# Kernel tuning notes

Measured on AMD Instinct MI355X. Metric: run time of the kernel, lower is better.

Reference implementation:

```python
import math
import jax, jax.numpy as jnp
import numpy as np

B, T, C, H = 4, 1024, 1024, 16
HD = C // H
BLOCK = 1024


def setup_inputs() -> dict:
    key = jax.random.key(0)
    k0, k1, k2, k3 = jax.random.split(key, 4)
    x = jax.random.normal(k0, (B, T, C), dtype=jnp.float32)
    # torch Linear weight is (out, in); we store (in, out) and apply x @ W + b
    W_attn = jax.random.normal(k1, (C, 3 * C), dtype=jnp.float32) * 0.02
    b_attn = jnp.zeros((3 * C,), dtype=jnp.float32)
    W_proj = jax.random.normal(k2, (C, C), dtype=jnp.float32) * 0.02
    b_proj = jnp.zeros((C,), dtype=jnp.float32)
    # rel_pos_emb: (n_head, block_size, head_dim), std 0.02 (leading 1 dim dropped)
    rel_pos_emb = jax.random.normal(k3, (H, BLOCK, HD), dtype=jnp.float32) * 0.02
    return {"x": x, "W_attn": W_attn, "b_attn": b_attn,
            "W_proj": W_proj, "b_proj": b_proj, "rel_pos_emb": rel_pos_emb}


def reference(x, W_attn, b_attn, W_proj, b_proj, rel_pos_emb):
    Bx, Tx, Cx = x.shape
    qkv = x @ W_attn + b_attn                      # (B, T, 3C)
    q, k, v = jnp.split(qkv, 3, axis=2)
    q = q.reshape(Bx, Tx, H, HD).transpose(0, 2, 1, 3)   # (B, H, T, hd)
    k = k.reshape(Bx, Tx, H, HD).transpose(0, 2, 1, 3)
    v = v.reshape(Bx, Tx, H, HD).transpose(0, 2, 1, 3)

    att = jnp.einsum('bhid,bhjd->bhij', q, k)      # (B, H, T, T)

    # relative position score: pos[b,h,i,j] = sum_d E[h, clamp(i-j,0), d] * k[b,h,j,d]
    # compute P[b,h,r,j] = <E[h,r,:], k[b,h,j,:]> then gather r = clamp(i-j, 0)
    rng = jnp.arange(Tx)
    dist = jnp.clip(rng[:, None] - rng[None, :], 0, None)          # (T, T)
    P = jnp.einsum('hrd,bhjd->bhrj', rel_pos_emb[:, :Tx], k)       # (B, H, T, T)
    pos_score = jnp.take_along_axis(P, dist[None, None, :, :], axis=2)
    att = att + pos_score

    att = att * (1.0 / math.sqrt(HD))
    causal = jnp.tril(jnp.ones((Tx, Tx), dtype=bool))
    att = jnp.where(causal[None, None], att, -jnp.inf)
    att = jax.nn.softmax(att, axis=-1)
    # dropout p=0.0 -> identity
    y = jnp.einsum('bhij,bhjd->bhid', att, v)      # (B, H, T, hd)
    y = y.transpose(0, 2, 1, 3).reshape(Bx, Tx, Cx)
    return y @ W_proj + b_proj
```

## Files before the change

### kernel.cpp

```cpp
#include <hip/hip_runtime.h>


typedef __bf16 bf16x8 __attribute__((ext_vector_type(8)));
typedef float f32x4 __attribute__((ext_vector_type(4)));
typedef unsigned short ushort_t;

#define T_SEQ 1024
#define NHEAD 16
#define HDIM 64
#define PLANE 4194304

__device__ __forceinline__ float bf2f(ushort_t h) {
    unsigned int u = ((unsigned int)h) << 16;
    float f; __builtin_memcpy(&f, &u, 4); return f;
}
__device__ __forceinline__ ushort_t f2bf(float f) {
    __bf16 h = (__bf16)f;
    ushort_t u; __builtin_memcpy(&u, &h, 2); return u;
}

__global__ __launch_bounds__(256) void sentinel_kernel(float* out, int n, float val) {
    const int i = blockIdx.x * 256 + threadIdx.x;
    if (i < n) out[i] = val;
}

__global__ __launch_bounds__(256) void convert2(
    const float* __restrict__ x, ushort_t* __restrict__ x16,
    const float* __restrict__ E, ushort_t* __restrict__ E16)
{
    const int bid = blockIdx.x;
    const float* src; ushort_t* dst; int base;
    if (bid < 4096) { src = x; dst = x16; base = bid * 1024; }
    else            { src = E; dst = E16; base = (bid - 4096) * 1024; }
    const int i = base + (int)threadIdx.x * 4;
    const float4 v = *reinterpret_cast<const float4*>(src + i);
    union { unsigned long long u; ushort_t s[4]; } o;
    o.s[0] = f2bf(v.x); o.s[1] = f2bf(v.y); o.s[2] = f2bf(v.z); o.s[3] = f2bf(v.w);
    *reinterpret_cast<unsigned long long*>(dst + i) = o.u;
}

__global__ __launch_bounds__(256) void transpose_bf16(
    const float* __restrict__ W, ushort_t* __restrict__ Wt, int Kdim, int Ndim)
{
    __shared__ ushort_t t[64][65];
    const int n0 = blockIdx.x * 64, k0 = blockIdx.y * 64;
    const int cx = threadIdx.x & 63, ry = threadIdx.x >> 6;
#pragma unroll
    for (int i = 0; i < 16; i++) {
        const int r = ry + i * 4;
        t[r][cx] = f2bf(W[(size_t)(k0 + r) * Ndim + n0 + cx]);
    }
    __syncthreads();
#pragma unroll
    for (int i = 0; i < 16; i++) {
        const int r = ry + i * 4;
        Wt[(size_t)(n0 + r) * Kdim + k0 + cx] = t[cx][r];
    }
}

__global__ __launch_bounds__(256) void transpose_v(
    const ushort_t* __restrict__ v, ushort_t* __restrict__ vT)
{
    __shared__ ushort_t t[64][65];
    const int bh = blockIdx.y;
    const int t0 = blockIdx.x * 64;
    const int cx = threadIdx.x & 63, ry = threadIdx.x >> 6;
    const ushort_t* src = v + (size_t)bh * 65536;
    ushort_t* dst = vT + (size_t)bh * 65536;
#pragma unroll
    for (int i = 0; i < 16; i++) {
        const int r = ry + i * 4;
        t[r][cx] = src[(size_t)(t0 + r) * HDIM + cx];
    }
    __syncthreads();
#pragma unroll
    for (int i = 0; i < 16; i++) {
        const int d = ry + i * 4;
        dst[(size_t)d * T_SEQ + t0 + cx] = t[cx][d];
    }
}

template <int MODE>
__global__ __launch_bounds__(256) void gemm128(
    const ushort_t* __restrict__ A16, const ushort_t* __restrict__ Bt,
    const float* __restrict__ bias, void* __restrict__ out_,
    int Ndim, int Kdim)
{
    __shared__ __align__(16) ushort_t As[128 * 32];
    __shared__ __align__(16) ushort_t Bs[128 * 32];

    const int tid = threadIdx.x;
    const int w = tid >> 6;
    const int lane = tid & 63;
    const int l15 = lane & 15;
    const int quad = lane >> 4;
    const int m0 = blockIdx.y * 128, n0 = blockIdx.x * 128;
    const int wm = (w & 1) * 64, wn = (w >> 1) * 64;

    f32x4 acc[4][4];
#pragma unroll
    for (int mt = 0; mt < 4; mt++)
#pragma unroll
        for (int nt = 0; nt < 4; nt++) acc[mt][nt] = (f32x4){0.f, 0.f, 0.f, 0.f};

    for (int kk = 0; kk < Kdim; kk += 32) {
        __syncthreads();
#pragma unroll
        for (int t = 0; t < 2; t++) {
            const int chunk = w * 128 + t * 64 + lane;
            const int row = chunk >> 2, kc = (chunk & 3) * 8;
            __builtin_amdgcn_global_load_lds(
                (const __attribute__((address_space(1))) void*)
                    (A16 + (size_t)(m0 + row) * Kdim + kk + kc),
                (__attribute__((address_space(3))) void*)
                    (As + (size_t)(w * 128 + t * 64) * 8), 16, 0, 0);
            __builtin_amdgcn_global_load_lds(
                (const __attribute__((address_space(1))) void*)
                    (Bt + (size_t)(n0 + row) * Kdim + kk + kc),
                (__attribute__((address_space(3))) void*)
                    (Bs + (size_t)(w * 128 + t * 64) * 8), 16, 0, 0);
        }
        __syncthreads();

        bf16x8 af[4], bf[4];
#pragma unroll
        for (int mt = 0; mt < 4; mt++)
            af[mt] = *reinterpret_cast<const bf16x8*>(&As[(wm + mt * 16 + l15) * 32 + quad * 8]);
#pragma unroll
        for (int nt = 0; nt < 4; nt++)
            bf[nt] = *reinterpret_cast<const bf16x8*>(&Bs[(wn + nt * 16 + l15) * 32 + quad * 8]);
#pragma unroll
        for (int mt = 0; mt < 4; mt++)
#pragma unroll
            for (int nt = 0; nt < 4; nt++)
                acc[mt][nt] = __builtin_amdgcn_mfma_f32_16x16x32_bf16(
                    af[mt], bf[nt], acc[mt][nt], 0, 0, 0);
    }

#pragma unroll
    for (int mt = 0; mt < 4; mt++)
#pragma unroll
        for (int nt = 0; nt < 4; nt++) {
            const int n = n0 + wn + nt * 16 + l15;
            const float bv = bias[n];
#pragma unroll
            for (int r = 0; r < 4; r++) {
                const int m = m0 + wm + mt * 16 + quad * 4 + r;
                const float val = acc[mt][nt][r] + bv;
                if (MODE == 0) {
                    ushort_t* ws = (ushort_t*)out_;
                    const int which = n >> 10;
                    const size_t pl = (which == 2) ? 3 : which;
                    const int cc = n & 1023;
                    const int h = cc >> 6, d = cc & 63;
                    const int bb = m >> 10, t = m & 1023;
                    ws[pl * PLANE + ((size_t)(bb * NHEAD + h) * T_SEQ + t) * HDIM + d] = f2bf(val);
                } else {
                    ((float*)out_)[(size_t)m * Ndim + n] = val;
                }
            }
        }
}

__global__ __launch_bounds__(256) void flash_attn(
    const ushort_t* __restrict__ qp, const ushort_t* __restrict__ kp,
    const ushort_t* __restrict__ vTp, const ushort_t* __restrict__ E16,
    ushort_t* __restrict__ y16)
{
    __shared__ __align__(16) ushort_t Ks[64 * 72];
    __shared__ __align__(16) ushort_t Vt[64 * 72];
    __shared__ __align__(16) ushort_t Es[128 * 72];
    __shared__ __align__(16) ushort_t Ps[64 * 68 + 16];

    const int bh = blockIdx.x;
    const int h = bh & (NHEAD - 1);
    const int b = bh >> 4;
    const int it = 15 - (int)blockIdx.y;
    const int tid = threadIdx.x;
    const int w = tid >> 6;
    const int lane = tid & 63;
    const int l15 = lane & 15;
    const int quad = lane >> 4;

    const size_t base = (size_t)bh * T_SEQ * HDIM;
    const ushort_t* Eh = E16 + (size_t)h * T_SEQ * HDIM;
    const ushort_t* vTb = vTp + (size_t)bh * 65536;
    const float c1 = 0.125f * 1.44269504f;

    const int rq = tid >> 2, cq = (tid & 3) * 16;
    const int re = tid >> 1, ce = (tid & 1) * 32;

    const int kosz = ((l15 >> 3) & 1) << 3;
    const int pswz = ((quad >> 1) & 1) << 3;
    const int l15p = l15 ^ pswz;
    const int eswz = ((re >> 3) & 1) << 3;

    bf16x8 ones;
#pragma unroll
    for (int i = 0; i < 8; i++) ones[i] = (__bf16)1.0f;

    const int i0 = it * 64;

    bf16x8 qf[2];
    {
        const ushort_t* qrow = qp + base + (size_t)(i0 + w * 16 + l15) * HDIM;
        qf[0] = *reinterpret_cast<const bf16x8*>(qrow + quad * 8);
        qf[1] = *reinterpret_cast<const bf16x8*>(qrow + 32 + quad * 8);
    }

    f32x4 o[4], o5;
#pragma unroll
    for (int dt = 0; dt < 4; dt++) o[dt] = (f32x4){0.f, 0.f, 0.f, 0.f};
    o5 = (f32x4){0.f, 0.f, 0.f, 0.f};
    float mrow[4];
#pragma unroll
    for (int r = 0; r < 4; r++) mrow[r] = -3e38f;

    for (int j0 = 0; j0 <= i0; j0 += 64) {
        const int d0 = i0 - j0;
        __syncthreads();
        {
            const ushort_t* ksrc = kp + base + (size_t)(j0 + rq) * HDIM + cq;
            *reinterpret_cast<uint4*>(&Ks[rq * 72 + cq]) = *reinterpret_cast<const uint4*>(ksrc);
            *reinterpret_cast<uint4*>(&Ks[rq * 72 + cq + 8]) = *reinterpret_cast<const uint4*>(ksrc + 8);
            const ushort_t* vsrc = vTb + (size_t)rq * T_SEQ + j0 + cq;
            *reinterpret_cast<uint4*>(&Vt[rq * 72 + cq]) = *reinterpret_cast<const uint4*>(vsrc);
            *reinterpret_cast<uint4*>(&Vt[rq * 72 + cq + 8]) = *reinterpret_cast<const uint4*>(vsrc + 8);
        }
        {
            int g = d0 - 64 + re;
            g = g < 0 ? 0 : (g > 1023 ? 1023 : g);
            const ushort_t* esrc = Eh + (size_t)g * HDIM + ce;
#pragma unroll
            for (int q16 = 0; q16 < 4; q16++)
                *reinterpret_cast<uint4*>(&Es[re * 72 + ce + ((q16 * 8) ^ eswz)]) =
                    *reinterpret_cast<const uint4*>(esrc + q16 * 8);
        }
        __syncthreads();

        f32x4 s[4], pb[2][4];
#pragma unroll
        for (int nt = 0; nt < 4; nt++) {
            s[nt] = (f32x4){0.f, 0.f, 0.f, 0.f};
            pb[0][nt] = (f32x4){0.f, 0.f, 0.f, 0.f};
            pb[1][nt] = (f32x4){0.f, 0.f, 0.f, 0.f};
        }
#pragma unroll
        for (int ks = 0; ks < 2; ks++) {
            const int ko = ks * 32 + quad * 8;
            const bf16x8 ae0 = *reinterpret_cast<const bf16x8*>(&Es[(w * 32 + l15) * 72 + (ko ^ kosz)]);
            const bf16x8 ae1 = *reinterpret_cast<const bf16x8*>(&Es[(w * 32 + 16 + l15) * 72 + (ko ^ kosz)]);
#pragma unroll
            for (int nt = 0; nt < 4; nt++) {
                const bf16x8 bk = *reinterpret_cast<const bf16x8*>(&Ks[(nt * 16 + l15) * 72 + ko]);
                s[nt] = __builtin_amdgcn_mfma_f32_16x16x32_bf16(qf[ks], bk, s[nt], 0, 0, 0);
                pb[0][nt] = __builtin_amdgcn_mfma_f32_16x16x32_bf16(ae0, bk, pb[0][nt], 0, 0, 0);
                pb[1][nt] = __builtin_amdgcn_mfma_f32_16x16x32_bf16(ae1, bk, pb[1][nt], 0, 0, 0);
            }
        }
#pragma unroll
        for (int mf = 0; mf < 2; mf++)
#pragma unroll
            for (int nt = 0; nt < 4; nt++) {
                const int jl = nt * 16 + l15;
#pragma unroll
                for (int r = 0; r < 4; r++) {
                    const int br = w * 32 + mf * 16 + quad * 4 + r;
                    const int il_t = br - 64 + jl;
                    const int addr = ((unsigned)il_t < 64u) ? il_t * 68 + jl : 4352;
                    Ps[addr] = f2bf(pb[mf][nt][r]);
                }
            }
        __syncthreads();

        float pv[4][4], mnew[4];
#pragma unroll
        for (int r = 0; r < 4; r++) mnew[r] = mrow[r];
        const int il0 = w * 16 + quad * 4;
        if (j0 < i0) {
#pragma unroll
            for (int nt = 0; nt < 4; nt++) {
                const int jl = nt * 16 + l15;
#pragma unroll
                for (int r = 0; r < 4; r++) {
                    const float sv = (s[nt][r] + bf2f(Ps[(il0 + r) * 68 + jl])) * c1;
                    pv[nt][r] = sv;
                    mnew[r] = fmaxf(mnew[r], sv);
                }
            }
        } else {
#pragma unroll
            for (int nt = 0; nt < 4; nt++) {
                const int jl = nt * 16 + l15;
#pragma unroll
                for (int r = 0; r < 4; r++) {
                    const int il = il0 + r;
                    float sv = (s[nt][r] + bf2f(Ps[il * 68 + jl])) * c1;
                    if (jl > il) sv = -3e38f;
                    pv[nt][r] = sv;
                    mnew[r] = fmaxf(mnew[r], sv);
                }
            }
        }
#pragma unroll
        for (int r = 0; r < 4; r++)
#pragma unroll
            for (int off = 1; off < 16; off <<= 1)
                mnew[r] = fmaxf(mnew[r], __shfl_xor(mnew[r], off, 64));
        float alpha[4];
#pragma unroll
        for (int r = 0; r < 4; r++) {
            alpha[r] = exp2f(mrow[r] - mnew[r]);
            mrow[r] = mnew[r];
        }
#pragma unroll
        for (int nt = 0; nt < 4; nt++)
#pragma unroll
            for (int r = 0; r < 4; r++)
                pv[nt][r] = exp2f(pv[nt][r] - mnew[r]);
#pragma unroll
        for (int dt = 0; dt < 4; dt++)
#pragma unroll
            for (int r = 0; r < 4; r++) o[dt][r] *= alpha[r];
#pragma unroll
        for (int r = 0; r < 4; r++) o5[r] *= alpha[r];
#pragma unroll
        for (int nt = 0; nt < 4; nt++)
#pragma unroll
            for (int r = 0; r < 4; r++)
                Es[(w * 16 + quad * 4 + r) * 72 + nt * 16 + l15p] = f2bf(pv[nt][r]);

#pragma unroll
        for (int ks = 0; ks < 2; ks++) {
            const int ko = ks * 32 + quad * 8;
            const bf16x8 ap = *reinterpret_cast<const bf16x8*>(&Es[(w * 16 + l15) * 72 + (ko ^ kosz)]);
#pragma unroll
            for (int dt = 0; dt < 4; dt++) {
                const bf16x8 bv = *reinterpret_cast<const bf16x8*>(&Vt[(dt * 16 + l15) * 72 + ko]);
                o[dt] = __builtin_amdgcn_mfma_f32_16x16x32_bf16(ap, bv, o[dt], 0, 0, 0);
            }
            o5 = __builtin_amdgcn_mfma_f32_16x16x32_bf16(ap, ones, o5, 0, 0, 0);
        }
    }

    float inv[4];
#pragma unroll
    for (int r = 0; r < 4; r++) inv[r] = 1.0f / o5[r];
#pragma unroll
    for (int dt = 0; dt < 4; dt++)
#pragma unroll
        for (int r = 0; r < 4; r++) {
            const int il = w * 16 + quad * 4 + r;
            const int d = dt * 16 + l15;
            y16[((size_t)(b * T_SEQ + i0 + il)) * 1024 + h * 64 + d] = f2bf(o[dt][r] * inv[r]);
        }
}

extern "C" void kernel_launch(void* const* d_in, const int* in_sizes, int n_in,
                              void* d_out, int out_size, void* d_ws, size_t ws_size,
                              hipStream_t stream) {
    float* out = (float*)d_out;

    const void* x = nullptr; const void* Wa = nullptr; const void* ba = nullptr;
    const void* Wp = nullptr; const void* bp = nullptr; const void* E = nullptr;
    int anomaly = 0;
    if (n_in != 6) {
        anomaly = 2;
    } else {
        int c1M = 0;
        for (int i = 0; i < 6; i++) {
            const int s = in_sizes[i];
            if      (s == 4194304) x  = d_in[i];
            else if (s == 3145728) Wa = d_in[i];
            else if (s == 3072)    ba = d_in[i];
            else if (s == 1024)    bp = d_in[i];
            else if (s == 1048576) { if (c1M == 0) Wp = d_in[i]; else E = d_in[i]; c1M++; }
            else anomaly = 1;
        }
        if (!x || !Wa || !ba || !Wp || !bp || !E || c1M != 2) anomaly = 1;
    }
    if (!anomaly && out_size != 4194304) anomaly = 3;
    if (!anomaly && ws_size < (size_t)52428800) anomaly = 4;
    if (anomaly) {
        sentinel_kernel<<<(out_size + 255) / 256, 256, 0, stream>>>(out, out_size, 1000.0f * anomaly);
        return;
    }

    ushort_t* ws   = (ushort_t*)d_ws;
    ushort_t* qp   = ws;
    ushort_t* kp   = ws + (size_t)PLANE;
    ushort_t* vTp  = ws + (size_t)2 * PLANE;
    ushort_t* vtmp = ws + (size_t)3 * PLANE;
    ushort_t* y16  = vtmp;
    ushort_t* x16  = ws + (size_t)4 * PLANE;
    ushort_t* WaT  = ws + (size_t)5 * PLANE;
    ushort_t* WpT  = WaT + (size_t)3145728;
    ushort_t* E16  = WpT + (size_t)1048576;

    convert2<<<5120, 256, 0, stream>>>((const float*)x, x16, (const float*)E, E16);
    transpose_bf16<<<dim3(48, 16), 256, 0, stream>>>((const float*)Wa, WaT, 1024, 3072);
    transpose_bf16<<<dim3(16, 16), 256, 0, stream>>>((const float*)Wp, WpT, 1024, 1024);

    gemm128<0><<<dim3(24, 32), 256, 0, stream>>>(x16, WaT, (const float*)ba, (void*)ws, 3072, 1024);

    transpose_v<<<dim3(16, 64), 256, 0, stream>>>(vtmp, vTp);

    flash_attn<<<dim3(64, 16), 256, 0, stream>>>(qp, kp, vTp, E16, y16);

    gemm128<1><<<dim3(8, 32), 256, 0, stream>>>(y16, WpT, (const float*)bp, (void*)out, 1024, 1024);
}
```

Before: 219.1 us.

## Fuse prep kernels, swizzle attention LDS, narrow projection GEMM tiles, add setprio

Merges the three weight and activation conversion kernels into a single prep launch. In flash attention it replaces padded LDS strides (72/68) with unpadded 64-wide rows using XOR swizzles, and reuses the Ks buffer for the probability tile. It also adds s_setprio around the MFMA sections and a launch_bounds occupancy hint of 4. The output projection GEMM switches to 128x64 tiles so that 512 blocks are launched instead of 256. These changes aim to cut launch overhead, LDS footprint and bank conflicts, and to raise occupancy, at the risk of swizzle-index mistakes and register pressure.

```diff
diff --git a/kernel.cpp b/kernel.cpp
--- a/kernel.cpp
+++ b/kernel.cpp
@@ -24,26 +24,35 @@
     if (i < n) out[i] = val;
 }
 
-__global__ __launch_bounds__(256) void convert2(
+__global__ __launch_bounds__(256) void prep(
     const float* __restrict__ x, ushort_t* __restrict__ x16,
-    const float* __restrict__ E, ushort_t* __restrict__ E16)
-{
-    const int bid = blockIdx.x;
-    const float* src; ushort_t* dst; int base;
-    if (bid < 4096) { src = x; dst = x16; base = bid * 1024; }
-    else            { src = E; dst = E16; base = (bid - 4096) * 1024; }
-    const int i = base + (int)threadIdx.x * 4;
-    const float4 v = *reinterpret_cast<const float4*>(src + i);
-    union { unsigned long long u; ushort_t s[4]; } o;
-    o.s[0] = f2bf(v.x); o.s[1] = f2bf(v.y); o.s[2] = f2bf(v.z); o.s[3] = f2bf(v.w);
-    *reinterpret_cast<unsigned long long*>(dst + i) = o.u;
-}
-
-__global__ __launch_bounds__(256) void transpose_bf16(
-    const float* __restrict__ W, ushort_t* __restrict__ Wt, int Kdim, int Ndim)
+    const float* __restrict__ E, ushort_t* __restrict__ E16,
+    const float* __restrict__ Wa, ushort_t* __restrict__ WaT,
+    const float* __restrict__ Wp, ushort_t* __restrict__ WpT)
 {
     __shared__ ushort_t t[64][65];
-    const int n0 = blockIdx.x * 64, k0 = blockIdx.y * 64;
+    const int bid = blockIdx.x;
+    if (bid < 5120) {
+        const float* src; ushort_t* dst; int base;
+        if (bid < 4096) { src = x; dst = x16; base = bid * 1024; }
+        else            { src = E; dst = E16; base = (bid - 4096) * 1024; }
+        const int i = base + (int)threadIdx.x * 4;
+        const float4 v = *reinterpret_cast<const float4*>(src + i);
+        union { unsigned long long u; ushort_t s[4]; } o;
+        o.s[0] = f2bf(v.x); o.s[1] = f2bf(v.y); o.s[2] = f2bf(v.z); o.s[3] = f2bf(v.w);
+        *reinterpret_cast<unsigned long long*>(dst + i) = o.u;
+        return;
+    }
+    const float* W; ushort_t* Wt; int Kdim, Ndim, n0, k0;
+    if (bid < 5888) {
+        const int r = bid - 5120;
+        W = Wa; Wt = WaT; Kdim = 1024; Ndim = 3072;
+        n0 = (r % 48) * 64; k0 = (r / 48) * 64;
+    } else {
+        const int r = bid - 5888;
+        W = Wp; Wt = WpT; Kdim = 1024; Ndim = 1024;
+        n0 = (r % 16) * 64; k0 = (r / 16) * 64;
+    }
     const int cx = threadIdx.x & 63, ry = threadIdx.x >> 6;
 #pragma unroll
     for (int i = 0; i < 16; i++) {
@@ -80,28 +89,29 @@
     }
 }
 
-template <int MODE>
+template <int MODE, int BN>
 __global__ __launch_bounds__(256) void gemm128(
     const ushort_t* __restrict__ A16, const ushort_t* __restrict__ Bt,
     const float* __restrict__ bias, void* __restrict__ out_,
     int Ndim, int Kdim)
 {
+    constexpr int NT = BN / 32;
     __shared__ __align__(16) ushort_t As[128 * 32];
-    __shared__ __align__(16) ushort_t Bs[128 * 32];
+    __shared__ __align__(16) ushort_t Bs[BN * 32];
 
     const int tid = threadIdx.x;
     const int w = tid >> 6;
     const int lane = tid & 63;
     const int l15 = lane & 15;
     const int quad = lane >> 4;
-    const int m0 = blockIdx.y * 128, n0 = blockIdx.x * 128;
-    const int wm = (w & 1) * 64, wn = (w >> 1) * 64;
-
-    f32x4 acc[4][4];
+    const int m0 = blockIdx.y * 128, n0 = blockIdx.x * BN;
+    const int wm = (w & 1) * 64, wn = (w >> 1) * (BN / 2);
+
+    f32x4 acc[4][NT];
 #pragma unroll
     for (int mt = 0; mt < 4; mt++)
 #pragma unroll
-        for (int nt = 0; nt < 4; nt++) acc[mt][nt] = (f32x4){0.f, 0.f, 0.f, 0.f};
+        for (int nt = 0; nt < NT; nt++) acc[mt][nt] = (f32x4){0.f, 0.f, 0.f, 0.f};
 
     for (int kk = 0; kk < Kdim; kk += 32) {
         __syncthreads();
@@ -114,25 +124,35 @@
                     (A16 + (size_t)(m0 + row) * Kdim + kk + kc),
                 (__attribute__((address_space(3))) void*)
                     (As + (size_t)(w * 128 + t * 64) * 8), 16, 0, 0);
+            if (BN == 128)
+                __builtin_amdgcn_global_load_lds(
+                    (const __attribute__((address_space(1))) void*)
+                        (Bt + (size_t)(n0 + row) * Kdim + kk + kc),
+                    (__attribute__((address_space(3))) void*)
+                        (Bs + (size_t)(w * 128 + t * 64) * 8), 16, 0, 0);
+        }
+        if (BN == 64) {
+            const int chunk = w * 64 + lane;
+            const int row = chunk >> 2, kc = (chunk & 3) * 8;
             __builtin_amdgcn_global_load_lds(
                 (const __attribute__((address_space(1))) void*)
                     (Bt + (size_t)(n0 + row) * Kdim + kk + kc),
                 (__attribute__((address_space(3))) void*)
-                    (Bs + (size_t)(w * 128 + t * 64) * 8), 16, 0, 0);
+                    (Bs + (size_t)(w * 64) * 8), 16, 0, 0);
         }
         __syncthreads();
 
-        bf16x8 af[4], bf[4];
+        bf16x8 af[4], bf[NT];
 #pragma unroll
         for (int mt = 0; mt < 4; mt++)
             af[mt] = *reinterpret_cast<const bf16x8*>(&As[(wm + mt * 16 + l15) * 32 + quad * 8]);
 #pragma unroll
-        for (int nt = 0; nt < 4; nt++)
+        for (int nt = 0; nt < NT; nt++)
             bf[nt] = *reinterpret_cast<const bf16x8*>(&Bs[(wn + nt * 16 + l15) * 32 + quad * 8]);
 #pragma unroll
         for (int mt = 0; mt < 4; mt++)
 #pragma unroll
-            for (int nt = 0; nt < 4; nt++)
+            for (int nt = 0; nt < NT; nt++)
                 acc[mt][nt] = __builtin_amdgcn_mfma_f32_16x16x32_bf16(
                     af[mt], bf[nt], acc[mt][nt], 0, 0, 0);
     }
@@ -140,7 +160,7 @@
 #pragma unroll
     for (int mt = 0; mt < 4; mt++)
 #pragma unroll
-        for (int nt = 0; nt < 4; nt++) {
+        for (int nt = 0; nt < NT; nt++) {
             const int n = n0 + wn + nt * 16 + l15;
             const float bv = bias[n];
 #pragma unroll
@@ -162,15 +182,15 @@
         }
 }
 
-__global__ __launch_bounds__(256) void flash_attn(
+__global__ __launch_bounds__(256, 4) void flash_attn(
     const ushort_t* __restrict__ qp, const ushort_t* __restrict__ kp,
     const ushort_t* __restrict__ vTp, const ushort_t* __restrict__ E16,
     ushort_t* __restrict__ y16)
 {
-    __shared__ __align__(16) ushort_t Ks[64 * 72];
-    __shared__ __align__(16) ushort_t Vt[64 * 72];
-    __shared__ __align__(16) ushort_t Es[128 * 72];
-    __shared__ __align__(16) ushort_t Ps[64 * 68 + 16];
+    __shared__ __align__(16) ushort_t Ks[64 * 64];
+    __shared__ __align__(16) ushort_t Vt[64 * 64];
+    __shared__ __align__(16) ushort_t Es[128 * 64];
+    __shared__ __align__(16) ushort_t Ps[64 * 64];
 
     const int bh = blockIdx.x;
     const int h = bh & (NHEAD - 1);
@@ -190,10 +210,10 @@
     const int rq = tid >> 2, cq = (tid & 3) * 16;
     const int re = tid >> 1, ce = (tid & 1) * 32;
 
-    const int kosz = ((l15 >> 3) & 1) << 3;
-    const int pswz = ((quad >> 1) & 1) << 3;
-    const int l15p = l15 ^ pswz;
-    const int eswz = ((re >> 3) & 1) << 3;
+    const int kswz = (l15 & 7) << 3;
+    const int swr  = (rq & 7) << 3;
+    const int swe  = (re & 7) << 3;
+    const int jswz = quad << 4;
 
     bf16x8 ones;
 #pragma unroll
@@ -221,11 +241,11 @@
         __syncthreads();
         {
             const ushort_t* ksrc = kp + base + (size_t)(j0 + rq) * HDIM + cq;
-            *reinterpret_cast<uint4*>(&Ks[rq * 72 + cq]) = *reinterpret_cast<const uint4*>(ksrc);
-            *reinterpret_cast<uint4*>(&Ks[rq * 72 + cq + 8]) = *reinterpret_cast<const uint4*>(ksrc + 8);
+            *reinterpret_cast<uint4*>(&Ks[rq * 64 + (cq ^ swr)]) = *reinterpret_cast<const uint4*>(ksrc);
+            *reinterpret_cast<uint4*>(&Ks[rq * 64 + ((cq + 8) ^ swr)]) = *reinterpret_cast<const uint4*>(ksrc + 8);
             const ushort_t* vsrc = vTb + (size_t)rq * T_SEQ + j0 + cq;
-            *reinterpret_cast<uint4*>(&Vt[rq * 72 + cq]) = *reinterpret_cast<const uint4*>(vsrc);
-            *reinterpret_cast<uint4*>(&Vt[rq * 72 + cq + 8]) = *reinterpret_cast<const uint4*>(vsrc + 8);
+            *reinterpret_cast<uint4*>(&Vt[rq * 64 + (cq ^ swr)]) = *reinterpret_cast<const uint4*>(vsrc);
+            *reinterpret_cast<uint4*>(&Vt[rq * 64 + ((cq + 8) ^ swr)]) = *reinterpret_cast<const uint4*>(vsrc + 8);
         }
         {
             int g = d0 - 64 + re;
@@ -233,7 +253,7 @@
             const ushort_t* esrc = Eh + (size_t)g * HDIM + ce;
 #pragma unroll
             for (int q16 = 0; q16 < 4; q16++)
-                *reinterpret_cast<uint4*>(&Es[re * 72 + ce + ((q16 * 8) ^ eswz)]) =
+                *reinterpret_cast<uint4*>(&Es[re * 64 + ((ce + q16 * 8) ^ swe)]) =
                     *reinterpret_cast<const uint4*>(esrc + q16 * 8);
         }
         __syncthreads();
@@ -245,19 +265,21 @@
             pb[0][nt] = (f32x4){0.f, 0.f, 0.f, 0.f};
             pb[1][nt] = (f32x4){0.f, 0.f, 0.f, 0.f};
         }
+        __builtin_amdgcn_s_setprio(1);
 #pragma unroll
         for (int ks = 0; ks < 2; ks++) {
             const int ko = ks * 32 + quad * 8;
-            const bf16x8 ae0 = *reinterpret_cast<const bf16x8*>(&Es[(w * 32 + l15) * 72 + (ko ^ kosz)]);
-            const bf16x8 ae1 = *reinterpret_cast<const bf16x8*>(&Es[(w * 32 + 16 + l15) * 72 + (ko ^ kosz)]);
+            const bf16x8 ae0 = *reinterpret_cast<const bf16x8*>(&Es[(w * 32 + l15) * 64 + (ko ^ kswz)]);
+            const bf16x8 ae1 = *reinterpret_cast<const bf16x8*>(&Es[(w * 32 + 16 + l15) * 64 + (ko ^ kswz)]);
 #pragma unroll
             for (int nt = 0; nt < 4; nt++) {
-                const bf16x8 bk = *reinterpret_cast<const bf16x8*>(&Ks[(nt * 16 + l15) * 72 + ko]);
+                const bf16x8 bk = *reinterpret_cast<const bf16x8*>(&Ks[(nt * 16 + l15) * 64 + (ko ^ kswz)]);
                 s[nt] = __builtin_amdgcn_mfma_f32_16x16x32_bf16(qf[ks], bk, s[nt], 0, 0, 0);
                 pb[0][nt] = __builtin_amdgcn_mfma_f32_16x16x32_bf16(ae0, bk, pb[0][nt], 0, 0, 0);
                 pb[1][nt] = __builtin_amdgcn_mfma_f32_16x16x32_bf16(ae1, bk, pb[1][nt], 0, 0, 0);
             }
         }
+        __builtin_amdgcn_s_setprio(0);
 #pragma unroll
         for (int mf = 0; mf < 2; mf++)
 #pragma unroll
@@ -267,8 +289,8 @@
                 for (int r = 0; r < 4; r++) {
                     const int br = w * 32 + mf * 16 + quad * 4 + r;
                     const int il_t = br - 64 + jl;
-                    const int addr = ((unsigned)il_t < 64u) ? il_t * 68 + jl : 4352;
-                    Ps[addr] = f2bf(pb[mf][nt][r]);
+                    if ((unsigned)il_t < 64u)
+                        Ps[il_t * 64 + (jl ^ (((il_t >> 2) & 3) << 4))] = f2bf(pb[mf][nt][r]);
                 }
             }
         __syncthreads();
@@ -283,7 +305,7 @@
                 const int jl = nt * 16 + l15;
 #pragma unroll
                 for (int r = 0; r < 4; r++) {
-                    const float sv = (s[nt][r] + bf2f(Ps[(il0 + r) * 68 + jl])) * c1;
+                    const float sv = (s[nt][r] + bf2f(Ps[(il0 + r) * 64 + (jl ^ jswz)])) * c1;
                     pv[nt][r] = sv;
                     mnew[r] = fmaxf(mnew[r], sv);
                 }
@@ -295,7 +317,7 @@
 #pragma unroll
                 for (int r = 0; r < 4; r++) {
                     const int il = il0 + r;
-                    float sv = (s[nt][r] + bf2f(Ps[il * 68 + jl])) * c1;
+                    float sv = (s[nt][r] + bf2f(Ps[il * 64 + (jl ^ jswz)])) * c1;
                     if (jl > il) sv = -3e38f;
                     pv[nt][r] = sv;
                     mnew[r] = fmaxf(mnew[r], sv);
@@ -327,20 +349,24 @@
 #pragma unroll
         for (int nt = 0; nt < 4; nt++)
 #pragma unroll
-            for (int r = 0; r < 4; r++)
-                Es[(w * 16 + quad * 4 + r) * 72 + nt * 16 + l15p] = f2bf(pv[nt][r]);
-
+            for (int r = 0; r < 4; r++) {
+                const int rr = w * 16 + quad * 4 + r;
+                Ks[rr * 64 + ((nt * 16 + l15) ^ ((rr & 7) << 3))] = f2bf(pv[nt][r]);
+            }
+
+        __builtin_amdgcn_s_setprio(1);
 #pragma unroll
         for (int ks = 0; ks < 2; ks++) {
             const int ko = ks * 32 + quad * 8;
-            const bf16x8 ap = *reinterpret_cast<const bf16x8*>(&Es[(w * 16 + l15) * 72 + (ko ^ kosz)]);
+            const bf16x8 ap = *reinterpret_cast<const bf16x8*>(&Ks[(w * 16 + l15) * 64 + (ko ^ kswz)]);
 #pragma unroll
             for (int dt = 0; dt < 4; dt++) {
-                const bf16x8 bv = *reinterpret_cast<const bf16x8*>(&Vt[(dt * 16 + l15) * 72 + ko]);
+                const bf16x8 bv = *reinterpret_cast<const bf16x8*>(&Vt[(dt * 16 + l15) * 64 + (ko ^ kswz)]);
                 o[dt] = __builtin_amdgcn_mfma_f32_16x16x32_bf16(ap, bv, o[dt], 0, 0, 0);
             }
             o5 = __builtin_amdgcn_mfma_f32_16x16x32_bf16(ap, ones, o5, 0, 0, 0);
         }
+        __builtin_amdgcn_s_setprio(0);
     }
 
     float inv[4];
@@ -397,15 +423,14 @@
     ushort_t* WpT  = WaT + (size_t)3145728;
     ushort_t* E16  = WpT + (size_t)1048576;
 
-    convert2<<<5120, 256, 0, stream>>>((const float*)x, x16, (const float*)E, E16);
-    transpose_bf16<<<dim3(48, 16), 256, 0, stream>>>((const float*)Wa, WaT, 1024, 3072);
-    transpose_bf16<<<dim3(16, 16), 256, 0, stream>>>((const float*)Wp, WpT, 1024, 1024);
-
-    gemm128<0><<<dim3(24, 32), 256, 0, stream>>>(x16, WaT, (const float*)ba, (void*)ws, 3072, 1024);
+    prep<<<6144, 256, 0, stream>>>((const float*)x, x16, (const float*)E, E16,
+                                   (const float*)Wa, WaT, (const float*)Wp, WpT);
+
+    gemm128<0, 128><<<dim3(24, 32), 256, 0, stream>>>(x16, WaT, (const float*)ba, (void*)ws, 3072, 1024);
 
     transpose_v<<<dim3(16, 64), 256, 0, stream>>>(vtmp, vTp);
 
     flash_attn<<<dim3(64, 16), 256, 0, stream>>>(qp, kp, vTp, E16, y16);
 
-    gemm128<1><<<dim3(8, 32), 256, 0, stream>>>(y16, WpT, (const float*)bp, (void*)out, 1024, 1024);
-}
+    gemm128<1, 64><<<dim3(16, 32), 256, 0, stream>>>(y16, WpT, (const float*)bp, (void*)out, 1024, 1024);
+}
```

After: 383.4 us. 1.75x slower.
